# Performance work log

Hardware: AMD Instinct MI355X
Metric: run time of the kernel (lower is better)

Reference implementation:

```python
import jax, jax.numpy as jnp
import numpy as np

DIM = 512
HEADS = 8
HEAD_DIM = DIM // HEADS
MLP = 2048
EPS = 1e-5


def _layer_norm(x, g, b):
    mu = jnp.mean(x, axis=-1, keepdims=True)
    var = jnp.var(x, axis=-1, keepdims=True)
    return (x - mu) * jax.lax.rsqrt(var + EPS) * g + b


def setup_inputs() -> dict:
    key = jax.random.key(0)
    ks = jax.random.split(key, 12)
    s = 1.0 / np.sqrt(DIM)
    sm = 1.0 / np.sqrt(MLP)
    return {
        "x": jax.random.normal(ks[0], (2, 4096, DIM), dtype=jnp.float32),
        "Wq": jax.random.normal(ks[1], (DIM, DIM), dtype=jnp.float32) * s,
        "Wk": jax.random.normal(ks[2], (DIM, DIM), dtype=jnp.float32) * s,
        "Wv": jax.random.normal(ks[3], (DIM, DIM), dtype=jnp.float32) * s,
        "Wo": jax.random.normal(ks[4], (DIM, DIM), dtype=jnp.float32) * s,
        "bo": jnp.zeros((DIM,), dtype=jnp.float32),
        "W1": jax.random.normal(ks[5], (DIM, MLP), dtype=jnp.float32) * s,
        "b1": jnp.zeros((MLP,), dtype=jnp.float32),
        "W2": jax.random.normal(ks[6], (MLP, DIM), dtype=jnp.float32) * sm,
        "b2": jnp.zeros((DIM,), dtype=jnp.float32),
        "g1": jnp.ones((DIM,), dtype=jnp.float32),
        "be1": jnp.zeros((DIM,), dtype=jnp.float32),
        "g2": jnp.ones((DIM,), dtype=jnp.float32),
        "be2": jnp.zeros((DIM,), dtype=jnp.float32),
    }


def reference(x, Wq, Wk, Wv, Wo, bo, W1, b1, W2, b2, g1, be1, g2, be2):
    b, n, d = x.shape
    # --- pre-norm multi-head attention ---
    h = _layer_norm(x, g1, be1)
    q = (h @ Wq).reshape(b, n, HEADS, HEAD_DIM).transpose(0, 2, 1, 3)  # [b,h,n,hd]
    k = (h @ Wk).reshape(b, n, HEADS, HEAD_DIM).transpose(0, 2, 1, 3)
    v = (h @ Wv).reshape(b, n, HEADS, HEAD_DIM).transpose(0, 2, 1, 3)
    scores = jnp.einsum("bhqd,bhkd->bhqk", q, k) / np.sqrt(HEAD_DIM)  # [b,h,n,n]
    attn = jax.nn.softmax(scores, axis=-1)
    out = jnp.einsum("bhqk,bhkd->bhqd", attn, v)
    out = out.transpose(0, 2, 1, 3).reshape(b, n, d)
    x = x + out @ Wo + bo
    # --- pre-norm feed-forward ---
    h2 = _layer_norm(x, g2, be2)
    ff = jax.nn.gelu(h2 @ W1 + b1, approximate=False) @ W2 + b2
    return x + ff
```

## Files before the change

### kernel.cpp

```cpp
#include <hip/hip_runtime.h>
#include <math.h>

#define BB   2
#define SEQ  4096
#define DIM  512
#define NH   8
#define HD   64
#define MLPD 2048
#define ROWS (BB*SEQ)
#define SZ   (ROWS*DIM)
#define EPSV 1e-5f

typedef __attribute__((ext_vector_type(8))) short bf16x8;
typedef __attribute__((ext_vector_type(4))) float f32x4;

#if __has_builtin(__builtin_amdgcn_exp2f)
#define EXP2(x) __builtin_amdgcn_exp2f(x)
#else
#define EXP2(x) exp2f(x)
#endif

__device__ __forceinline__ ushort f2bf(float f) {
    unsigned u = __float_as_uint(f);
    u += 0x7fffu + ((u >> 16) & 1u);
    return (ushort)(u >> 16);
}
__device__ __forceinline__ unsigned pack2bf(float a, float b) {
    return (unsigned)f2bf(a) | ((unsigned)f2bf(b) << 16);
}
__device__ __forceinline__ unsigned pack2bf_tr(float a, float b) {
    return (__float_as_uint(a) >> 16) | (__float_as_uint(b) & 0xffff0000u);
}

__device__ __forceinline__ void gload16(const ushort* g, ushort* l) {
    __builtin_amdgcn_global_load_lds(
        (const __attribute__((address_space(1))) unsigned*)g,
        (__attribute__((address_space(3))) unsigned*)l, 16, 0, 0);
}

__global__ __launch_bounds__(128) void ln_kernel(const float* __restrict__ x,
        const float* __restrict__ g, const float* __restrict__ be,
        ushort* __restrict__ out)
{
    int row = blockIdx.x;
    int tid = threadIdx.x;
    const float4 v = ((const float4*)(x + (size_t)row*DIM))[tid];
    float s  = v.x + v.y + v.z + v.w;
    float ss = v.x*v.x + v.y*v.y + v.z*v.z + v.w*v.w;
    #pragma unroll
    for (int off = 32; off > 0; off >>= 1) {
        s  += __shfl_down(s,  off);
        ss += __shfl_down(ss, off);
    }
    __shared__ float red[4];
    if ((tid & 63) == 0) { red[(tid>>6)*2+0] = s; red[(tid>>6)*2+1] = ss; }
    __syncthreads();
    float sum = red[0] + red[2], sumsq = red[1] + red[3];
    float mu  = sum * (1.0f/DIM);
    float var = sumsq * (1.0f/DIM) - mu*mu;
    float rs  = rsqrtf(var + EPSV);
    float4 gv = ((const float4*)g)[tid];
    float4 bv = ((const float4*)be)[tid];
    ushort4 o;
    o.x = f2bf((v.x - mu)*rs*gv.x + bv.x);
    o.y = f2bf((v.y - mu)*rs*gv.y + bv.y);
    o.z = f2bf((v.z - mu)*rs*gv.z + bv.z);
    o.w = f2bf((v.w - mu)*rs*gv.w + bv.w);
    ((ushort4*)(out + (size_t)row*DIM))[tid] = o;
}

__global__ __launch_bounds__(256) void wtrans_kernel(const float* __restrict__ W,
        ushort* __restrict__ Wt, int K, int N)
{
    __shared__ ushort T[64][65];
    int n0 = blockIdx.x*64, k0 = blockIdx.y*64;
    int tid = threadIdx.x;
    #pragma unroll
    for (int p = 0; p < 4; ++p) {
        int r = p*16 + (tid>>4), c = (tid&15)<<2;
        float4 w4 = *(const float4*)(W + (size_t)(k0+r)*N + n0 + c);
        T[c+0][r] = f2bf(w4.x); T[c+1][r] = f2bf(w4.y);
        T[c+2][r] = f2bf(w4.z); T[c+3][r] = f2bf(w4.w);
    }
    __syncthreads();
    #pragma unroll
    for (int p = 0; p < 4; ++p) {
        int n = p*16 + (tid>>4), k = (tid&15)<<2;
        ushort4 o; o.x = T[n][k]; o.y = T[n][k+1]; o.z = T[n][k+2]; o.w = T[n][k+3];
        *(ushort4*)(Wt + (size_t)(n0+n)*K + k0 + k) = o;
    }
}

__global__ __launch_bounds__(256) void wtrans4_kernel(
        const float* __restrict__ W0, const float* __restrict__ W1,
        const float* __restrict__ W2, const float* __restrict__ W3,
        ushort* __restrict__ Wt)
{
    __shared__ ushort T[64][65];
    int z = blockIdx.z;
    const float* W = (z==0) ? W0 : (z==1) ? W1 : (z==2) ? W2 : W3;
    ushort* Wtz = Wt + (size_t)z*512*512;
    int n0 = blockIdx.x*64, k0 = blockIdx.y*64;
    int tid = threadIdx.x;
    #pragma unroll
    for (int p = 0; p < 4; ++p) {
        int r = p*16 + (tid>>4), c = (tid&15)<<2;
        float4 w4 = *(const float4*)(W + (size_t)(k0+r)*512 + n0 + c);
        T[c+0][r] = f2bf(w4.x); T[c+1][r] = f2bf(w4.y);
        T[c+2][r] = f2bf(w4.z); T[c+3][r] = f2bf(w4.w);
    }
    __syncthreads();
    #pragma unroll
    for (int p = 0; p < 4; ++p) {
        int n = p*16 + (tid>>4), k = (tid&15)<<2;
        ushort4 o; o.x = T[n][k]; o.y = T[n][k+1]; o.z = T[n][k+2]; o.w = T[n][k+3];
        *(ushort4*)(Wtz + (size_t)(n0+n)*512 + k0 + k) = o;
    }
}

template<int BM, int NT>
__global__ __launch_bounds__(NT) void gemm_bf16_kernel(
        const ushort* __restrict__ A,
        const ushort* __restrict__ Wta, const ushort* __restrict__ Wtb, const ushort* __restrict__ Wtc,
        const float* __restrict__ bias, const float* __restrict__ resid,
        void* __restrict__ outv, int M, int Nn, int K, int flags)
{
    constexpr int AISS = (BM*4)/NT;
    constexpr int BISS = 256/NT;
    __shared__ ushort As[2][BM*32];
    __shared__ ushort Bs[2][64*32];
    int tid = threadIdx.x;
    int w = tid >> 6, lane = tid & 63, quad = lane >> 4, col = lane & 15;
    int row0 = blockIdx.y * BM, col0 = blockIdx.x * 64;
    int wm0 = w * 32;

    const ushort* Wt; int wcol0, ostride, obase_col;
    float qscale = 1.0f;
    float* outF = nullptr; ushort* outB = nullptr;
    if (flags & 1) {
        int sel = col0 >> 9;
        Wt = (sel == 0) ? Wta : ((sel == 1) ? Wtb : Wtc);
        wcol0 = col0 & 511; ostride = 512; obase_col = wcol0;
        outB = (ushort*)outv + (size_t)sel * ((size_t)M * 512);
        if (sel == 0) qscale = 0.125f * 1.44269504088896f;
        flags |= 16;
    } else {
        Wt = Wta; wcol0 = col0; ostride = Nn; obase_col = col0;
        if (flags & 16) outB = (ushort*)outv; else outF = (float*)outv;
    }

    f32x4 acc[2][4];
    #pragma unroll
    for (int i = 0; i < 2; ++i)
        #pragma unroll
        for (int j = 0; j < 4; ++j) acc[i][j] = (f32x4){0.f,0.f,0.f,0.f};

    const ushort* Ag = A  + (size_t)(row0  + (tid >> 2))*K + ((tid & 3) << 3);
    const ushort* Bg = Wt + (size_t)(wcol0 + (tid >> 2))*K + ((tid & 3) << 3);

    auto issue = [&](ushort* Ad, ushort* Bd, int ko) {
        #pragma unroll
        for (int it = 0; it < AISS; ++it)
            gload16(Ag + ko + (size_t)(it*(NT/4))*K, Ad + it*NT*8 + tid*8);
        #pragma unroll
        for (int it = 0; it < BISS; ++it)
            gload16(Bg + ko + (size_t)(it*(NT/4))*K, Bd + it*NT*8 + tid*8);
    };
    auto compute = [&](const ushort* Ab, const ushort* Bb) {
        bf16x8 af[2], bfr[4];
        #pragma unroll
        for (int i = 0; i < 2; ++i)
            af[i] = *(const bf16x8*)(Ab + (wm0 + i*16 + col)*32 + quad*8);
        #pragma unroll
        for (int j = 0; j < 4; ++j)
            bfr[j] = *(const bf16x8*)(Bb + (j*16 + col)*32 + quad*8);
        #pragma unroll
        for (int i = 0; i < 2; ++i)
            #pragma unroll
            for (int j = 0; j < 4; ++j)
                acc[i][j] = __builtin_amdgcn_mfma_f32_16x16x32_bf16(af[i], bfr[j], acc[i][j], 0, 0, 0);
    };

    int niter = K >> 5;
    issue(As[0], Bs[0], 0);
    for (int i = 0; i < niter; i += 2) {
        __syncthreads();
        if (i + 1 < niter) issue(As[1], Bs[1], (i+1)*32);
        compute(As[0], Bs[0]);
        __syncthreads();
        if (i + 2 < niter) issue(As[0], Bs[0], (i+2)*32);
        compute(As[1], Bs[1]);
    }

    #pragma unroll
    for (int i = 0; i < 2; ++i) {
        #pragma unroll
        for (int r = 0; r < 4; ++r) {
            int row = row0 + wm0 + i*16 + quad*4 + r;
            #pragma unroll
            for (int j = 0; j < 4; ++j) {
                int oc = obase_col + j*16 + col;
                float o = acc[i][j][r] * qscale;
                if (flags & 8) o += bias[oc];
                if (flags & 2) o = 0.5f*o*(1.f + erff(o*0.70710678118654752f));
                if (flags & 4) o += resid[(size_t)row*ostride + oc];
                if (flags & 16) outB[(size_t)row*ostride + oc] = f2bf(o);
                else            outF[(size_t)row*ostride + oc] = o;
            }
        }
    }
}

__global__ __launch_bounds__(256) void vtrans_kernel(const ushort* __restrict__ v,
                                                     ushort* __restrict__ vt)
{
    int tt = blockIdx.x, bh = blockIdx.y;
    int b = bh >> 3, h = bh & 7;
    int tid = threadIdx.x;
    int d = tid >> 2, t0 = (tid & 3) << 4;
    ushort tmp[16];
    #pragma unroll
    for (int i = 0; i < 16; ++i) {
        int kp = t0 + i;
        int korig = ((kp>>5)*2 + ((kp>>2)&1))*16 + ((kp>>3)&3)*4 + (kp&3);
        tmp[i] = v[(size_t)(b*SEQ + tt*64 + korig)*DIM + h*HD + d];
    }
    unsigned u[8];
    #pragma unroll
    for (int j = 0; j < 8; ++j) u[j] = (unsigned)tmp[2*j] | ((unsigned)tmp[2*j+1] << 16);
    ushort* dst = vt + ((size_t)bh*HD + d)*SEQ + tt*64 + t0;
    *(uint4*)(dst)     = make_uint4(u[0],u[1],u[2],u[3]);
    *(uint4*)(dst + 8) = make_uint4(u[4],u[5],u[6],u[7]);
}

__global__ __launch_bounds__(256, 2) void attn_mfma_kernel(
        const ushort* __restrict__ q, const ushort* __restrict__ k,
        const ushort* __restrict__ vt, ushort* __restrict__ out)
{
    __shared__ __align__(16) ushort Kt[2][64][72];
    __shared__ __align__(16) ushort Vt[2][64][72];

    int qt = blockIdx.x, bh = blockIdx.y;
    int b = bh >> 3, h = bh & 7;
    int tid = threadIdx.x;
    int w = tid >> 6, lane = tid & 63;
    int quad = lane >> 4, col = lane & 15;
    int qw = w >> 1, kw = w & 1;
    int qn0 = qt*128 + qw*64;

    bf16x8 aq[4][2];
    #pragma unroll
    for (int mt = 0; mt < 4; ++mt) {
        const ushort* qp = q + (size_t)(b*SEQ + qn0 + mt*16 + col)*DIM + h*HD + quad*8;
        aq[mt][0] = *(const bf16x8*)(qp);
        aq[mt][1] = *(const bf16x8*)(qp + 32);
    }
    const short one_bf = (short)0x3F80;
    const bf16x8 ones = {one_bf,one_bf,one_bf,one_bf,one_bf,one_bf,one_bf,one_bf};
    const f32x4 zf = {0.f,0.f,0.f,0.f};

    f32x4 ot[4][4];
    f32x4 ol[4];
    #pragma unroll
    for (int mt = 0; mt < 4; ++mt) {
        ol[mt] = zf;
        #pragma unroll
        for (int t4 = 0; t4 < 4; ++t4) ot[mt][t4] = zf;
    }

    int skey = tid >> 2, sd0 = (tid & 3) << 4;
    bf16x8 kr[2], vr[2];
    auto load_tile = [&](int t) {
        const ushort* kp = k + (size_t)(b*SEQ + t*64 + skey)*DIM + h*HD + sd0;
        kr[0] = *(const bf16x8*)(kp);
        kr[1] = *(const bf16x8*)(kp + 8);
        const ushort* vp = vt + ((size_t)bh*HD + skey)*SEQ + t*64 + sd0;
        vr[0] = *(const bf16x8*)(vp);
        vr[1] = *(const bf16x8*)(vp + 8);
    };
    auto store_tile = [&](int p) {
        *(bf16x8*)&Kt[p][skey][sd0]     = kr[0];
        *(bf16x8*)&Kt[p][skey][sd0+8]   = kr[1];
        *(bf16x8*)&Vt[p][skey][sd0]     = vr[0];
        *(bf16x8*)&Vt[p][skey][sd0+8]   = vr[1];
    };

    load_tile(0);
    store_tile(0);
    __syncthreads();

    int krow0 = kw << 5;
    for (int t = 0; t < SEQ/64; ++t) {
        int p = t & 1;
        if (t + 1 < SEQ/64) load_tile(t + 1);

        bf16x8 kf0[2], kf1[2];
        #pragma unroll
        for (int kb = 0; kb < 2; ++kb) {
            const ushort* kbp = &Kt[p][krow0 + kb*16 + col][quad*8];
            kf0[kb] = *(const bf16x8*)(kbp);
            kf1[kb] = *(const bf16x8*)(kbp + 32);
        }
        f32x4 sc[4][2];
        #pragma unroll
        for (int mt = 0; mt < 4; ++mt)
            #pragma unroll
            for (int kb = 0; kb < 2; ++kb) {
                sc[mt][kb] = __builtin_amdgcn_mfma_f32_16x16x32_bf16(kf0[kb], aq[mt][0], zf, 0, 0, 0);
                sc[mt][kb] = __builtin_amdgcn_mfma_f32_16x16x32_bf16(kf1[kb], aq[mt][1], sc[mt][kb], 0, 0, 0);
            }

        union PU { bf16x8 v; uint4 u; };
        PU pb[4];
        #pragma unroll
        for (int mt = 0; mt < 4; ++mt) {
            pb[mt].u.x = pack2bf_tr(EXP2(sc[mt][0][0]), EXP2(sc[mt][0][1]));
            pb[mt].u.y = pack2bf_tr(EXP2(sc[mt][0][2]), EXP2(sc[mt][0][3]));
            pb[mt].u.z = pack2bf_tr(EXP2(sc[mt][1][0]), EXP2(sc[mt][1][1]));
            pb[mt].u.w = pack2bf_tr(EXP2(sc[mt][1][2]), EXP2(sc[mt][1][3]));
        }

        bf16x8 vf[4];
        #pragma unroll
        for (int t4 = 0; t4 < 4; ++t4)
            vf[t4] = *(const bf16x8*)&Vt[p][t4*16 + col][krow0 + quad*8];
        #pragma unroll
        for (int mt = 0; mt < 4; ++mt) {
            #pragma unroll
            for (int t4 = 0; t4 < 4; ++t4)
                ot[mt][t4] = __builtin_amdgcn_mfma_f32_16x16x32_bf16(vf[t4], pb[mt].v, ot[mt][t4], 0, 0, 0);
            ol[mt] = __builtin_amdgcn_mfma_f32_16x16x32_bf16(ones, pb[mt].v, ol[mt], 0, 0, 0);
        }

        if (t + 1 < SEQ/64) store_tile(p ^ 1);
        __syncthreads();
    }

    f32x4* redA = (f32x4*)Kt;
    f32x4* redB = (f32x4*)Vt;
    int rbase = ((qw << 6) + lane) * 9;
    if (kw) {
        #pragma unroll
        for (int t4 = 0; t4 < 4; ++t4) {
            redA[rbase + t4]     = ot[0][t4];
            redA[rbase + 4 + t4] = ot[1][t4];
            redB[rbase + t4]     = ot[2][t4];
            redB[rbase + 4 + t4] = ot[3][t4];
        }
        redA[rbase + 8] = (f32x4){ol[0][0], ol[1][0], ol[2][0], ol[3][0]};
    }
    __syncthreads();
    if (!kw) {
        f32x4 olp = redA[rbase + 8];
        #pragma unroll
        for (int mt = 0; mt < 4; ++mt) {
            float inv = 1.0f / (ol[mt][0] + olp[mt]);
            #pragma unroll
            for (int t4 = 0; t4 < 4; ++t4) {
                f32x4 r = (mt < 2) ? redA[rbase + mt*4 + t4]
                                   : redB[rbase + (mt-2)*4 + t4];
                f32x4 o = ot[mt][t4] + r;
                ushort4 o4;
                o4.x = f2bf(o[0] * inv);
                o4.y = f2bf(o[1] * inv);
                o4.z = f2bf(o[2] * inv);
                o4.w = f2bf(o[3] * inv);
                *(ushort4*)(out + (size_t)(b*SEQ + qn0 + mt*16 + col)*DIM + h*HD + t4*16 + quad*4) = o4;
            }
        }
    }
}

extern "C" void kernel_launch(void* const* d_in, const int* in_sizes, int n_in,
                              void* d_out, int out_size, void* d_ws, size_t ws_size,
                              hipStream_t stream)
{
    (void)in_sizes; (void)n_in; (void)out_size; (void)ws_size;
    const float* x   = (const float*)d_in[0];
    const float* Wq  = (const float*)d_in[1];
    const float* Wk  = (const float*)d_in[2];
    const float* Wv  = (const float*)d_in[3];
    const float* Wo  = (const float*)d_in[4];
    const float* bo  = (const float*)d_in[5];
    const float* W1  = (const float*)d_in[6];
    const float* b1  = (const float*)d_in[7];
    const float* W2  = (const float*)d_in[8];
    const float* b2  = (const float*)d_in[9];
    const float* g1  = (const float*)d_in[10];
    const float* be1 = (const float*)d_in[11];
    const float* g2  = (const float*)d_in[12];
    const float* be2 = (const float*)d_in[13];

    ushort* u = (ushort*)d_ws;
    float*  x2    = (float*)u;
    ushort* h     = u + 2*(size_t)SZ;
    ushort* qb    = u + 3*(size_t)SZ;
    ushort* kb    = u + 4*(size_t)SZ;
    ushort* vb    = u + 5*(size_t)SZ;
    ushort* vtb   = u + 6*(size_t)SZ;
    ushort* attnb = u + 7*(size_t)SZ;
    ushort* ff1   = u + 3*(size_t)SZ;
    ushort* wqkv  = u + 8*(size_t)SZ;
    ushort* wto   = wqkv + 3*(size_t)512*512;
    ushort* wt1   = wqkv + 4*(size_t)512*512;
    ushort* wt2   = wt1  + (size_t)512*2048;
    float*  outp  = (float*)d_out;

    wtrans4_kernel<<<dim3(8,8,4), 256, 0, stream>>>(Wq, Wk, Wv, Wo, wqkv);
    wtrans_kernel<<<dim3(32,8), 256, 0, stream>>>(W1, wt1, 512, 2048);
    wtrans_kernel<<<dim3(8,32), 256, 0, stream>>>(W2, wt2, 2048, 512);

    ln_kernel<<<ROWS, 128, 0, stream>>>(x, g1, be1, h);
    gemm_bf16_kernel<128,256><<<dim3(1536/64, ROWS/128), 256, 0, stream>>>(
        h, wqkv, wqkv + (size_t)512*512, wqkv + 2*(size_t)512*512,
        nullptr, nullptr, qb, ROWS, 1536, DIM, 1);
    vtrans_kernel<<<dim3(SEQ/64, BB*NH), 256, 0, stream>>>(vb, vtb);
    attn_mfma_kernel<<<dim3(SEQ/128, BB*NH), 256, 0, stream>>>(qb, kb, vtb, attnb);
    gemm_bf16_kernel<64,128><<<dim3(DIM/64, ROWS/64), 128, 0, stream>>>(
        attnb, wto, wto, wto, bo, x, x2, ROWS, DIM, DIM, 8|4);
    ln_kernel<<<ROWS, 128, 0, stream>>>(x2, g2, be2, h);
    gemm_bf16_kernel<128,256><<<dim3(MLPD/64, ROWS/128), 256, 0, stream>>>(
        h, wt1, wt1, wt1, b1, nullptr, ff1, ROWS, MLPD, DIM, 8|2|16);
    gemm_bf16_kernel<64,128><<<dim3(DIM/64, ROWS/64), 128, 0, stream>>>(
        ff1, wt2, wt2, wt2, b2, x2, outp, ROWS, DIM, MLPD, 8|4);
}
```

Measured before the change: 349.1 us.

## Load K/V MFMA fragments directly from global memory, dropping LDS staging

The attention kernel no longer stages K and V tiles through double-buffered shared memory with a block barrier per tile. Each wave now loads its MFMA fragments straight from global memory into registers, ping-ponging two register sets so the next tile's loads overlap the current tile's compute. This removes the LDS writes, LDS reads and per-iteration __syncthreads. In exchange, K and V data shared between the two query-half waves is fetched twice from global/L2, the access pattern is less coalesced, and register pressure rises.

```diff
diff --git a/kernel.cpp b/kernel.cpp
--- a/kernel.cpp
+++ b/kernel.cpp
@@ -237,8 +237,8 @@
         const ushort* __restrict__ q, const ushort* __restrict__ k,
         const ushort* __restrict__ vt, ushort* __restrict__ out)
 {
-    __shared__ __align__(16) ushort Kt[2][64][72];
-    __shared__ __align__(16) ushort Vt[2][64][72];
+    __shared__ f32x4 redA[1152];
+    __shared__ f32x4 redB[1152];
 
     int qt = blockIdx.x, bh = blockIdx.y;
     int b = bh >> 3, h = bh & 7;
@@ -247,6 +247,7 @@
     int quad = lane >> 4, col = lane & 15;
     int qw = w >> 1, kw = w & 1;
     int qn0 = qt*128 + qw*64;
+    int krow0 = kw << 5;
 
     bf16x8 aq[4][2];
     #pragma unroll
@@ -268,76 +269,54 @@
         for (int t4 = 0; t4 < 4; ++t4) ot[mt][t4] = zf;
     }
 
-    int skey = tid >> 2, sd0 = (tid & 3) << 4;
-    bf16x8 kr[2], vr[2];
-    auto load_tile = [&](int t) {
-        const ushort* kp = k + (size_t)(b*SEQ + t*64 + skey)*DIM + h*HD + sd0;
-        kr[0] = *(const bf16x8*)(kp);
-        kr[1] = *(const bf16x8*)(kp + 8);
-        const ushort* vp = vt + ((size_t)bh*HD + skey)*SEQ + t*64 + sd0;
-        vr[0] = *(const bf16x8*)(vp);
-        vr[1] = *(const bf16x8*)(vp + 8);
+    const ushort* kp0 = k  + (size_t)(b*SEQ + krow0 + col)*DIM + h*HD + quad*8;
+    const ushort* vp0 = vt + ((size_t)bh*HD + col)*SEQ + krow0 + quad*8;
+
+    auto load_frags = [&](bf16x8 (&kfb)[2][2], bf16x8 (&vfb)[4], int t) {
+        const ushort* kpt = kp0 + (size_t)t*(64*DIM);
+        kfb[0][0] = *(const bf16x8*)(kpt);
+        kfb[0][1] = *(const bf16x8*)(kpt + 32);
+        kfb[1][0] = *(const bf16x8*)(kpt + 16*DIM);
+        kfb[1][1] = *(const bf16x8*)(kpt + 16*DIM + 32);
+        const ushort* vpt = vp0 + t*64;
+        vfb[0] = *(const bf16x8*)(vpt);
+        vfb[1] = *(const bf16x8*)(vpt + 16*SEQ);
+        vfb[2] = *(const bf16x8*)(vpt + 32*SEQ);
+        vfb[3] = *(const bf16x8*)(vpt + 48*SEQ);
     };
-    auto store_tile = [&](int p) {
-        *(bf16x8*)&Kt[p][skey][sd0]     = kr[0];
-        *(bf16x8*)&Kt[p][skey][sd0+8]   = kr[1];
-        *(bf16x8*)&Vt[p][skey][sd0]     = vr[0];
-        *(bf16x8*)&Vt[p][skey][sd0+8]   = vr[1];
-    };
-
-    load_tile(0);
-    store_tile(0);
-    __syncthreads();
-
-    int krow0 = kw << 5;
-    for (int t = 0; t < SEQ/64; ++t) {
-        int p = t & 1;
-        if (t + 1 < SEQ/64) load_tile(t + 1);
-
-        bf16x8 kf0[2], kf1[2];
-        #pragma unroll
-        for (int kb = 0; kb < 2; ++kb) {
-            const ushort* kbp = &Kt[p][krow0 + kb*16 + col][quad*8];
-            kf0[kb] = *(const bf16x8*)(kbp);
-            kf1[kb] = *(const bf16x8*)(kbp + 32);
-        }
+    auto compute = [&](const bf16x8 (&kfb)[2][2], const bf16x8 (&vfb)[4]) {
         f32x4 sc[4][2];
         #pragma unroll
         for (int mt = 0; mt < 4; ++mt)
             #pragma unroll
             for (int kb = 0; kb < 2; ++kb) {
-                sc[mt][kb] = __builtin_amdgcn_mfma_f32_16x16x32_bf16(kf0[kb], aq[mt][0], zf, 0, 0, 0);
-                sc[mt][kb] = __builtin_amdgcn_mfma_f32_16x16x32_bf16(kf1[kb], aq[mt][1], sc[mt][kb], 0, 0, 0);
+                sc[mt][kb] = __builtin_amdgcn_mfma_f32_16x16x32_bf16(kfb[kb][0], aq[mt][0], zf, 0, 0, 0);
+                sc[mt][kb] = __builtin_amdgcn_mfma_f32_16x16x32_bf16(kfb[kb][1], aq[mt][1], sc[mt][kb], 0, 0, 0);
             }
-
         union PU { bf16x8 v; uint4 u; };
-        PU pb[4];
         #pragma unroll
         for (int mt = 0; mt < 4; ++mt) {
-            pb[mt].u.x = pack2bf_tr(EXP2(sc[mt][0][0]), EXP2(sc[mt][0][1]));
-            pb[mt].u.y = pack2bf_tr(EXP2(sc[mt][0][2]), EXP2(sc[mt][0][3]));
-            pb[mt].u.z = pack2bf_tr(EXP2(sc[mt][1][0]), EXP2(sc[mt][1][1]));
-            pb[mt].u.w = pack2bf_tr(EXP2(sc[mt][1][2]), EXP2(sc[mt][1][3]));
-        }
-
-        bf16x8 vf[4];
-        #pragma unroll
-        for (int t4 = 0; t4 < 4; ++t4)
-            vf[t4] = *(const bf16x8*)&Vt[p][t4*16 + col][krow0 + quad*8];
-        #pragma unroll
-        for (int mt = 0; mt < 4; ++mt) {
+            PU pb;
+            pb.u.x = pack2bf_tr(EXP2(sc[mt][0][0]), EXP2(sc[mt][0][1]));
+            pb.u.y = pack2bf_tr(EXP2(sc[mt][0][2]), EXP2(sc[mt][0][3]));
+            pb.u.z = pack2bf_tr(EXP2(sc[mt][1][0]), EXP2(sc[mt][1][1]));
+            pb.u.w = pack2bf_tr(EXP2(sc[mt][1][2]), EXP2(sc[mt][1][3]));
             #pragma unroll
             for (int t4 = 0; t4 < 4; ++t4)
-                ot[mt][t4] = __builtin_amdgcn_mfma_f32_16x16x32_bf16(vf[t4], pb[mt].v, ot[mt][t4], 0, 0, 0);
-            ol[mt] = __builtin_amdgcn_mfma_f32_16x16x32_bf16(ones, pb[mt].v, ol[mt], 0, 0, 0);
+                ot[mt][t4] = __builtin_amdgcn_mfma_f32_16x16x32_bf16(vfb[t4], pb.v, ot[mt][t4], 0, 0, 0);
+            ol[mt] = __builtin_amdgcn_mfma_f32_16x16x32_bf16(ones, pb.v, ol[mt], 0, 0, 0);
         }
-
-        if (t + 1 < SEQ/64) store_tile(p ^ 1);
-        __syncthreads();
-    }
-
-    f32x4* redA = (f32x4*)Kt;
-    f32x4* redB = (f32x4*)Vt;
+    };
+
+    bf16x8 kfA[2][2], vfA[4], kfB[2][2], vfB[4];
+    load_frags(kfA, vfA, 0);
+    for (int t = 0; t < SEQ/64; t += 2) {
+        if (t + 1 < SEQ/64) load_frags(kfB, vfB, t + 1);
+        compute(kfA, vfA);
+        if (t + 2 < SEQ/64) load_frags(kfA, vfA, t + 2);
+        compute(kfB, vfB);
+    }
+
     int rbase = ((qw << 6) + lane) * 9;
     if (kw) {
         #pragma unroll
```

Result: slower. 402.9 us (+15.4%).
